# Optimization experiments

Hardware: AMD Instinct MI355X
Metric: run time of the kernel (lower is better)

The kernel has to match this reference:

```python
import jax, jax.numpy as jnp
import numpy as np

B, N = 4096, 64
EPS = 1e-6
LANE = np.array([13.55, 17.45, 21.12, 24.91], dtype=np.float32)


def _lin_params(key, out_f, in_f):
    k1, k2 = jax.random.split(key)
    bound = 1.0 / np.sqrt(in_f)
    W = jax.random.uniform(k1, (out_f, in_f), jnp.float32, -bound, bound)
    b = jax.random.uniform(k2, (out_f,), jnp.float32, -bound, bound)
    return W, b


def setup_inputs() -> dict:
    key = jax.random.key(0)
    ks = jax.random.split(key, 16)
    inp = {
        "ego_y": jax.random.uniform(ks[0], (B,), jnp.float32, 10.0, 28.0),
        "Pn": jax.random.normal(ks[1], (B, N, 2), jnp.float32),
        "Pego": jax.random.normal(ks[2], (B, 2), jnp.float32),
        "Vn": jax.random.normal(ks[3], (B, N, 2), jnp.float32),
        "Vego": jax.random.normal(ks[4], (B, 2), jnp.float32),
        "Cn": jax.random.normal(ks[5], (B, N, 2), jnp.float32),
    }
    inp["W_sel"], inp["b_sel"] = _lin_params(ks[6], 4, 4)
    inp["W_s0"], inp["b_s0"] = _lin_params(ks[7], 8, 4)      # aug_sin0
    inp["W_map"], inp["b_map"] = _lin_params(ks[8], 8, 48)   # Er map
    inp["W_efc"], inp["b_efc"] = _lin_params(ks[9], 2, 8)
    inp["W_s1"], inp["b_s1"] = _lin_params(ks[10], 17, 2)    # aug_sin1
    inp["W1"], inp["b1"] = _lin_params(ks[11], 256, 114)     # En_mlp
    inp["W2"], inp["b2"] = _lin_params(ks[12], 128, 256)
    inp["W3"], inp["b3"] = _lin_params(ks[13], 2, 128)
    inp["Ww"], inp["bw"] = _lin_params(ks[14], 1, 6)
    return inp


def _leaky(x):
    return jnp.where(x >= 0, x, 0.1 * x)


def _auge(data, W_sin, b_sin):
    # data: [..., d]; returns concat of 10 feature blocks along last axis
    sin = jnp.sin(data @ W_sin.T + b_sin) + EPS
    sqr = data ** 2 + EPS
    cub = data ** 3 + EPS
    exp = jnp.exp(data) + EPS
    inv = 1.0 / (data + EPS)
    return jnp.concatenate(
        [data, sin, sqr, cub, exp, inv, 1.0 / sin, 1.0 / sqr, 1.0 / cub, 1.0 / exp],
        axis=-1,
    )


def reference(ego_y, Pn, Pego, Vn, Vego, Cn,
              W_sel, b_sel, W_s0, b_s0, W_map, b_map, W_efc, b_efc,
              W_s1, b_s1, W1, b1, W2, b2, W3, b3, Ww, bw):
    lane = jnp.asarray(LANE)
    # ---- Er_net (batched over B) ----
    delta_y = lane[None, :] - ego_y[:, None]                      # [B,4]
    x = jax.nn.softmax(delta_y @ W_sel.T + b_sel, axis=-1) * delta_y
    x = _auge(x, W_s0, b_s0)                                      # [B,48]
    x = _leaky(x @ W_map.T + b_map)                               # [B,8]
    Er = x @ W_efc.T + b_efc                                      # [B,2]

    # ---- En_net (batched over B, vectorized over N neighbors) ----
    Pego_r = jnp.broadcast_to(Pego[:, None, :], (B, N, 2))
    Vego_r = jnp.broadcast_to(Vego[:, None, :], (B, N, 2))
    dP = Pn - Pego_r
    dV = Vn - Vego_r
    dP_aug = _auge(dP, W_s1, b_s1)                                # [B,N,50]
    dV_aug = _auge(dV, W_s1, b_s1)                                # [B,N,50]
    Ninfo = jnp.concatenate(
        [Pego_r, Pn, dP, dP_aug, Vego_r, Vn, dV, dV_aug, Cn], axis=-1
    )                                                             # [B,N,114]
    h = _leaky(Ninfo @ W1.T + b1)                                 # [B,N,256]
    h = _leaky(h @ W2.T + b2)                                     # [B,N,128]
    En = h @ W3.T + b3                                            # [B,N,2]
    logits = jnp.concatenate([En, Pn, dP], axis=-1) @ Ww.T + bw   # [B,N,1]
    weight = jax.nn.softmax(logits, axis=1)                       # softmax over neighbors
    En_out = jnp.sum(weight * En, axis=1)                         # [B,2]

    return jnp.concatenate([Er, En_out], axis=-1)                 # [B,4]
```

## Files before the change

kernel.cpp:

```cpp
#include <hip/hip_runtime.h>
#include <math.h>

#define EPS 1e-6f
#define NB 4096
#define NN 64

typedef __attribute__((ext_vector_type(8))) short short8_t;
typedef __attribute__((ext_vector_type(4))) short short4_t;
typedef __attribute__((ext_vector_type(4))) float f32x4;

__device__ __forceinline__ unsigned short f2bf(float x) {
  unsigned u = __float_as_uint(x);
  u = u + 0x7fffu + ((u >> 16) & 1u);
  return (unsigned short)(u >> 16);
}

__global__ __launch_bounds__(512)
void w_prep_kernel(const float* __restrict__ W1,
                   const float* __restrict__ W2,
                   short* __restrict__ W1F,
                   short* __restrict__ W2F) {
  __shared__ float S[32768];
  const int tid = threadIdx.x;
  if (blockIdx.x == 0) {
    for (int i = tid; i < 256 * 114; i += 512) S[i] = W1[i];
    __syncthreads();
    for (int u = tid; u < 4096; u += 512) {
      int l = u & 63, ks = (u >> 6) & 3, mt = u >> 8;
      int m = mt * 16 + (l & 15);
      int k0 = ks * 32 + (l >> 4) * 8;
      short8_t hi, lo;
#pragma unroll
      for (int j = 0; j < 8; j++) {
        int k = k0 + j;
        float x = (k < 114) ? S[m * 114 + k] : 0.0f;
        unsigned uu = __float_as_uint(x);
        hi[j] = (short)(unsigned short)(uu >> 16);
        lo[j] = (short)f2bf(x - __uint_as_float(uu & 0xFFFF0000u));
      }
      int base = ((mt * 4 + ks) * 64 + l) * 8;
      *(short8_t*)&W1F[base] = hi;
      *(short8_t*)&W1F[32768 + base] = lo;
    }
  } else {
    for (int i = tid; i < 128 * 256; i += 512) S[i] = W2[i];
    __syncthreads();
    for (int u = tid; u < 4096; u += 512) {
      int l = u & 63, ks = (u >> 6) & 7, mt = u >> 9;
      int m = mt * 16 + (l & 15);
      int k0 = ks * 32 + (l >> 4) * 8;
      short8_t hi, lo;
#pragma unroll
      for (int j = 0; j < 8; j++) {
        float x = S[m * 256 + k0 + j];
        unsigned uu = __float_as_uint(x);
        hi[j] = (short)(unsigned short)(uu >> 16);
        lo[j] = (short)f2bf(x - __uint_as_float(uu & 0xFFFF0000u));
      }
      int base = ((mt * 8 + ks) * 64 + l) * 8;
      *(short8_t*)&W2F[base] = hi;
      *(short8_t*)&W2F[32768 + base] = lo;
    }
  }
}

__global__ __launch_bounds__(512, 4)
void en_kernel(const float* __restrict__ Pn, const float* __restrict__ Pego,
               const float* __restrict__ Vn, const float* __restrict__ Vego,
               const float* __restrict__ Cn,
               const float* __restrict__ W_s1, const float* __restrict__ b_s1,
               const float* __restrict__ b1, const float* __restrict__ b2,
               const float* __restrict__ W3, const float* __restrict__ b3,
               const float* __restrict__ Ww, const float* __restrict__ bw,
               const float* __restrict__ ego_y,
               const float* __restrict__ W_sel, const float* __restrict__ b_sel,
               const float* __restrict__ W_s0, const float* __restrict__ b_s0,
               const float* __restrict__ W_map, const float* __restrict__ b_map,
               const float* __restrict__ W_efc, const float* __restrict__ b_efc,
               const short* __restrict__ W1F, const short* __restrict__ W2F,
               float* __restrict__ out) {
  __shared__ __align__(16) short uni[2][64 * 256];
  __shared__ float stash[4 * 64];
  __shared__ float w3s[256];
  __shared__ float en_part[4][64][2];

  const int b = blockIdx.x;
  const int tid = threadIdx.x;
  const int w = tid >> 6;
  const int l = tid & 63;
  const int lr = l & 15;
  const int lq = l >> 4;
  const int ntb = (w >> 2) * 2;

  if (tid < 256) w3s[tid] = W3[tid];

  {
    const int r = l;
    const int rsw = (r & 7) << 3;
    auto putg = [&](int g, const float* v) {
      short8_t hi, lo;
#pragma unroll
      for (int i = 0; i < 8; i++) {
        unsigned u = __float_as_uint(v[i]);
        hi[i] = (short)(unsigned short)(u >> 16);
        lo[i] = (short)f2bf(v[i] - __uint_as_float(u & 0xFFFF0000u));
      }
      int idx = r * 128 + ((g * 8) ^ rsw);
      *(short8_t*)&uni[0][idx] = hi;
      *(short8_t*)&uni[1][idx] = lo;
    };
    if (w == 6) {
      const float2 p2 = ((const float2*)Pn)[b * NN + r];
      float e0 = Pego[b * 2 + 0], e1 = Pego[b * 2 + 1];
      stash[0 * 64 + r] = p2.x; stash[1 * 64 + r] = p2.y;
      stash[2 * 64 + r] = p2.x - e0; stash[3 * 64 + r] = p2.y - e1;
      const float2 cn = ((const float2*)Cn)[b * NN + r];
      float g14[8] = {cn.x, cn.y, 0.f, 0.f, 0.f, 0.f, 0.f, 0.f};
      float g15[8] = {0.f, 0.f, 0.f, 0.f, 0.f, 0.f, 0.f, 0.f};
      putg(14, g14);
      putg(15, g15);
    } else if (w < 6) {
      const bool isV = (w >= 3);
      const int role = isV ? (w - 3) : w;
      const int gb = isV ? 7 : 0;
      const float2 p2 = ((const float2*)(isV ? Vn : Pn))[b * NN + r];
      const float* Eb = isV ? Vego : Pego;
      float e0 = Eb[b * 2 + 0], e1 = Eb[b * 2 + 1];
      float d0 = p2.x - e0, d1 = p2.y - e1;
      if (role == 0) {
        float a15 = fmaf(W_s1[30], d0, fmaf(W_s1[31], d1, b_s1[15]));
        float a16 = fmaf(W_s1[32], d0, fmaf(W_s1[33], d1, b_s1[16]));
        float s15 = sinf(a15) + EPS, s16 = sinf(a16) + EPS;
        float q0 = d0 * d0 + EPS, q1 = d1 * d1 + EPS;
        float c30 = (d0 * d0) * d0 + EPS, c31 = (d1 * d1) * d1 + EPS;
        float ex0 = expf(d0) + EPS, ex1 = expf(d1) + EPS;
        float g0[8] = {e0, e1, p2.x, p2.y, d0, d1, d0, d1};
        float g3[8] = {s16, q0, q1, c30, c31, ex0, ex1, 1.0f / (d0 + EPS)};
        float g6[8] = {1.0f / s15, 1.0f / s16, 1.0f / q0, 1.0f / q1,
                       1.0f / c30, 1.0f / c31, 1.0f / ex0, 1.0f / ex1};
        putg(gb + 0, g0);
        putg(gb + 3, g3);
        putg(gb + 6, g6);
      } else if (role == 1) {
        float s[8];
#pragma unroll
        for (int i = 0; i < 8; i++) {
          float a = fmaf(W_s1[2 * i], d0, fmaf(W_s1[2 * i + 1], d1, b_s1[i]));
          s[i] = sinf(a) + EPS;
        }
        float g1[8] = {s[0], s[1], s[2], s[3], s[4], s[5], s[6], s[7]};
        float g4[8] = {1.0f / (d1 + EPS), 1.0f / s[0], 1.0f / s[1], 1.0f / s[2],
                       1.0f / s[3], 1.0f / s[4], 1.0f / s[5], 1.0f / s[6]};
        putg(gb + 1, g1);
        putg(gb + 4, g4);
      } else {
        float s[9];
#pragma unroll
        for (int i = 0; i < 9; i++) {
          float a = fmaf(W_s1[2 * (7 + i)], d0,
                         fmaf(W_s1[2 * (7 + i) + 1], d1, b_s1[7 + i]));
          s[i] = sinf(a) + EPS;
        }
        float g2[8] = {s[1], s[2], s[3], s[4], s[5], s[6], s[7], s[8]};
        float g5[8] = {1.0f / s[0], 1.0f / s[1], 1.0f / s[2], 1.0f / s[3],
                       1.0f / s[4], 1.0f / s[5], 1.0f / s[6], 1.0f / s[7]};
        putg(gb + 2, g2);
        putg(gb + 5, g5);
      }
    } else if (l < 8) {
      const int sub = l;
      const float lane4[4] = {13.55f, 17.45f, 21.12f, 24.91f};
      float ego = ego_y[b];
      float dy[4];
#pragma unroll
      for (int j = 0; j < 4; j++) dy[j] = lane4[j] - ego;
      float t[4];
#pragma unroll
      for (int i = 0; i < 4; i++) {
        float a = b_sel[i];
#pragma unroll
        for (int j = 0; j < 4; j++) a = fmaf(W_sel[i * 4 + j], dy[j], a);
        t[i] = a;
      }
      float m = fmaxf(fmaxf(t[0], t[1]), fmaxf(t[2], t[3]));
      float e[4], s = 0.f;
#pragma unroll
      for (int i = 0; i < 4; i++) { e[i] = expf(t[i] - m); s += e[i]; }
      float x[4];
#pragma unroll
      for (int i = 0; i < 4; i++) x[i] = (e[i] / s) * dy[i];
      float f[48];
      float sn[8];
#pragma unroll
      for (int k = 0; k < 8; k++) {
        float a = b_s0[k];
#pragma unroll
        for (int j = 0; j < 4; j++) a = fmaf(W_s0[k * 4 + j], x[j], a);
        sn[k] = sinf(a) + EPS;
      }
#pragma unroll
      for (int i = 0; i < 4; i++) f[i] = x[i];
#pragma unroll
      for (int k = 0; k < 8; k++) f[4 + k] = sn[k];
#pragma unroll
      for (int i = 0; i < 4; i++) {
        float q = x[i] * x[i] + EPS;
        f[12 + i] = q; f[36 + i] = 1.0f / q;
      }
#pragma unroll
      for (int i = 0; i < 4; i++) {
        float c3 = (x[i] * x[i]) * x[i] + EPS;
        f[16 + i] = c3; f[40 + i] = 1.0f / c3;
      }
#pragma unroll
      for (int i = 0; i < 4; i++) {
        float ex = expf(x[i]) + EPS;
        f[20 + i] = ex; f[44 + i] = 1.0f / ex;
      }
#pragma unroll
      for (int i = 0; i < 4; i++) f[24 + i] = 1.0f / (x[i] + EPS);
#pragma unroll
      for (int k = 0; k < 8; k++) f[28 + k] = 1.0f / sn[k];
      float a = b_map[sub];
#pragma unroll
      for (int k = 0; k < 48; k++) a = fmaf(W_map[sub * 48 + k], f[k], a);
      float y = fmaxf(a, 0.1f * a);
      float t0 = W_efc[sub] * y;
      float t1 = W_efc[8 + sub] * y;
#pragma unroll
      for (int off = 4; off > 0; off >>= 1) {
        t0 += __shfl_xor(t0, off);
        t1 += __shfl_xor(t1, off);
      }
      if (sub == 0) {
        out[b * 4 + 0] = t0 + b_efc[0];
        out[b * 4 + 1] = t1 + b_efc[1];
      }
    }
  }
  __syncthreads();

  const short* w1b = W1F + (w & 3) * 4 * 4 * 512 + l * 8;
  f32x4 acc1[4][2];
#pragma unroll
  for (int m = 0; m < 4; m++)
#pragma unroll
    for (int n = 0; n < 2; n++) acc1[m][n] = (f32x4)0.0f;

#pragma unroll
  for (int ks = 0; ks < 4; ks++) {
    short8_t w1h[4], w1l[4];
#pragma unroll
    for (int m = 0; m < 4; m++) {
      w1h[m] = *(const short8_t*)&w1b[(m * 4 + ks) * 512];
      w1l[m] = *(const short8_t*)&w1b[32768 + (m * 4 + ks) * 512];
    }
    short8_t bh[2], bl[2];
#pragma unroll
    for (int n = 0; n < 2; n++) {
      int rr = (ntb + n) * 16 + lr;
      int idx = rr * 128 + ((ks * 32 + lq * 8) ^ ((rr & 7) << 3));
      bh[n] = *(const short8_t*)&uni[0][idx];
      bl[n] = *(const short8_t*)&uni[1][idx];
    }
    __builtin_amdgcn_s_setprio(1);
#pragma unroll
    for (int m = 0; m < 4; m++)
#pragma unroll
      for (int n = 0; n < 2; n++)
        acc1[m][n] = __builtin_amdgcn_mfma_f32_16x16x32_bf16(
            w1h[m], bh[n], acc1[m][n], 0, 0, 0);
#pragma unroll
    for (int m = 0; m < 4; m++)
#pragma unroll
      for (int n = 0; n < 2; n++)
        acc1[m][n] = __builtin_amdgcn_mfma_f32_16x16x32_bf16(
            w1h[m], bl[n], acc1[m][n], 0, 0, 0);
#pragma unroll
    for (int m = 0; m < 4; m++)
#pragma unroll
      for (int n = 0; n < 2; n++)
        acc1[m][n] = __builtin_amdgcn_mfma_f32_16x16x32_bf16(
            w1l[m], bh[n], acc1[m][n], 0, 0, 0);
    __builtin_amdgcn_s_setprio(0);
  }

  __syncthreads();

#pragma unroll
  for (int m = 0; m < 4; m++) {
    int o0 = ((w & 3) * 4 + m) * 16 + lq * 4;
    f32x4 bb = *(const f32x4*)&b1[o0];
#pragma unroll
    for (int n = 0; n < 2; n++) {
      int rr = (ntb + n) * 16 + lr;
      short4_t hq, lo4;
#pragma unroll
      for (int i = 0; i < 4; i++) {
        float v = acc1[m][n][i] + bb[i];
        v = fmaxf(v, 0.1f * v);
        unsigned u = __float_as_uint(v);
        hq[i] = (short)(unsigned short)(u >> 16);
        lo4[i] = (short)f2bf(v - __uint_as_float(u & 0xFFFF0000u));
      }
      int idx = rr * 256 + (o0 ^ ((rr & 7) << 3));
      *(short4_t*)&uni[0][idx] = hq;
      *(short4_t*)&uni[1][idx] = lo4;
    }
  }
  __syncthreads();

  const short* w2b = W2F + (w & 3) * 2 * 8 * 512 + l * 8;
  f32x4 acc2[2][2];
#pragma unroll
  for (int m = 0; m < 2; m++)
#pragma unroll
    for (int n = 0; n < 2; n++) acc2[m][n] = (f32x4)0.0f;

#pragma unroll
  for (int ks = 0; ks < 8; ks++) {
    short8_t w2h[2], w2l[2];
#pragma unroll
    for (int m = 0; m < 2; m++) {
      w2h[m] = *(const short8_t*)&w2b[(m * 8 + ks) * 512];
      w2l[m] = *(const short8_t*)&w2b[32768 + (m * 8 + ks) * 512];
    }
    short8_t bh[2], bl[2];
#pragma unroll
    for (int n = 0; n < 2; n++) {
      int rr = (ntb + n) * 16 + lr;
      int idx = rr * 256 + ((ks * 32 + lq * 8) ^ ((rr & 7) << 3));
      bh[n] = *(const short8_t*)&uni[0][idx];
      bl[n] = *(const short8_t*)&uni[1][idx];
    }
    __builtin_amdgcn_s_setprio(1);
#pragma unroll
    for (int m = 0; m < 2; m++)
#pragma unroll
      for (int n = 0; n < 2; n++)
        acc2[m][n] = __builtin_amdgcn_mfma_f32_16x16x32_bf16(
            w2h[m], bh[n], acc2[m][n], 0, 0, 0);
#pragma unroll
    for (int m = 0; m < 2; m++)
#pragma unroll
      for (int n = 0; n < 2; n++)
        acc2[m][n] = __builtin_amdgcn_mfma_f32_16x16x32_bf16(
            w2h[m], bl[n], acc2[m][n], 0, 0, 0);
#pragma unroll
    for (int m = 0; m < 2; m++)
#pragma unroll
      for (int n = 0; n < 2; n++)
        acc2[m][n] = __builtin_amdgcn_mfma_f32_16x16x32_bf16(
            w2l[m], bh[n], acc2[m][n], 0, 0, 0);
    __builtin_amdgcn_s_setprio(0);
  }

  {
    f32x4 w3v[2][2];
#pragma unroll
    for (int c = 0; c < 2; c++)
#pragma unroll
      for (int m = 0; m < 2; m++)
        w3v[c][m] = *(const f32x4*)
            &w3s[c * 128 + ((w & 3) * 2 + m) * 16 + lq * 4];

    float p00 = 0.f, p01 = 0.f, p10 = 0.f, p11 = 0.f;
#pragma unroll
    for (int m = 0; m < 2; m++) {
      int o0 = ((w & 3) * 2 + m) * 16 + lq * 4;
      f32x4 bb = *(const f32x4*)&b2[o0];
#pragma unroll
      for (int i = 0; i < 4; i++) {
        float u0 = acc2[m][0][i] + bb[i];
        u0 = fmaxf(u0, 0.1f * u0);
        float u1 = acc2[m][1][i] + bb[i];
        u1 = fmaxf(u1, 0.1f * u1);
        p00 = fmaf(u0, w3v[0][m][i], p00);
        p10 = fmaf(u0, w3v[1][m][i], p10);
        p01 = fmaf(u1, w3v[0][m][i], p01);
        p11 = fmaf(u1, w3v[1][m][i], p11);
      }
    }
#pragma unroll
    for (int off = 16; off < 64; off <<= 1) {
      p00 += __shfl_xor(p00, off);
      p01 += __shfl_xor(p01, off);
      p10 += __shfl_xor(p10, off);
      p11 += __shfl_xor(p11, off);
    }
    if (l < 16) {
      en_part[w & 3][ntb * 16 + l][0] = p00;
      en_part[w & 3][ntb * 16 + l][1] = p10;
      en_part[w & 3][(ntb + 1) * 16 + l][0] = p01;
      en_part[w & 3][(ntb + 1) * 16 + l][1] = p11;
    }
  }
  __syncthreads();

  if (tid < 64) {
    const int r = tid;
    float E0 = b3[0] + en_part[0][r][0] + en_part[1][r][0] +
               en_part[2][r][0] + en_part[3][r][0];
    float E1 = b3[1] + en_part[0][r][1] + en_part[1][r][1] +
               en_part[2][r][1] + en_part[3][r][1];
    float pn0 = stash[0 * 64 + r], pn1 = stash[1 * 64 + r];
    float dp0 = stash[2 * 64 + r], dp1 = stash[3 * 64 + r];
    float logit = bw[0];
    logit = fmaf(E0, Ww[0], logit);
    logit = fmaf(E1, Ww[1], logit);
    logit = fmaf(pn0, Ww[2], logit);
    logit = fmaf(pn1, Ww[3], logit);
    logit = fmaf(dp0, Ww[4], logit);
    logit = fmaf(dp1, Ww[5], logit);
    float m = logit;
#pragma unroll
    for (int off = 32; off > 0; off >>= 1) m = fmaxf(m, __shfl_xor(m, off));
    float e = expf(logit - m);
    float ssum = e;
#pragma unroll
    for (int off = 32; off > 0; off >>= 1) ssum += __shfl_xor(ssum, off);
    float wgt = e / ssum;
    float o0 = wgt * E0, o1 = wgt * E1;
#pragma unroll
    for (int off = 32; off > 0; off >>= 1) {
      o0 += __shfl_xor(o0, off);
      o1 += __shfl_xor(o1, off);
    }
    if (r == 0) {
      out[b * 4 + 2] = o0;
      out[b * 4 + 3] = o1;
    }
  }
}

extern "C" void kernel_launch(void* const* d_in, const int* in_sizes, int n_in,
                              void* d_out, int out_size, void* d_ws, size_t ws_size,
                              hipStream_t stream) {
  const float* ego_y = (const float*)d_in[0];
  const float* Pn    = (const float*)d_in[1];
  const float* Pego  = (const float*)d_in[2];
  const float* Vn    = (const float*)d_in[3];
  const float* Vego  = (const float*)d_in[4];
  const float* Cn    = (const float*)d_in[5];
  const float* W_sel = (const float*)d_in[6];
  const float* b_sel = (const float*)d_in[7];
  const float* W_s0  = (const float*)d_in[8];
  const float* b_s0  = (const float*)d_in[9];
  const float* W_map = (const float*)d_in[10];
  const float* b_map = (const float*)d_in[11];
  const float* W_efc = (const float*)d_in[12];
  const float* b_efc = (const float*)d_in[13];
  const float* W_s1  = (const float*)d_in[14];
  const float* b_s1  = (const float*)d_in[15];
  const float* W1    = (const float*)d_in[16];
  const float* b1    = (const float*)d_in[17];
  const float* W2    = (const float*)d_in[18];
  const float* b2    = (const float*)d_in[19];
  const float* W3    = (const float*)d_in[20];
  const float* b3    = (const float*)d_in[21];
  const float* Ww    = (const float*)d_in[22];
  const float* bw    = (const float*)d_in[23];
  float* out = (float*)d_out;

  short* W1F = (short*)d_ws;
  short* W2F = W1F + 65536;

  w_prep_kernel<<<2, 512, 0, stream>>>(W1, W2, W1F, W2F);
  en_kernel<<<NB, 512, 0, stream>>>(Pn, Pego, Vn, Vego, Cn, W_s1, b_s1,
                                    b1, b2, W3, b3, Ww, bw,
                                    ego_y, W_sel, b_sel, W_s0, b_s0,
                                    W_map, b_map, W_efc, b_efc,
                                    W1F, W2F, out);
}
```

Before: 218.0 us.

## Switch MLP GEMMs to 32x32x16 MFMA tiles and parallelize weight prep

Both hidden-layer GEMMs now use 32x32x16 bf16 MFMA instead of 16x16x32. Each wave handles a 32-row neighbor tile against 64 or 32 output features, and the weight fragment layout in the prep kernel is rebuilt to match. The prep kernel is split across 12 blocks instead of 2 so weight packing no longer serializes on two blocks. Biases b1/b2 are staged in shared memory, and the final reduction shrinks to one cross-half shuffle. The larger tiles cut LDS operand reads and MFMA instruction count, at the cost of larger accumulator register use.

Result: slower. 232.2 us (+6.5%).

```diff
diff --git a/kernel.cpp b/kernel.cpp
--- a/kernel.cpp
+++ b/kernel.cpp
@@ -8,6 +8,7 @@
 typedef __attribute__((ext_vector_type(8))) short short8_t;
 typedef __attribute__((ext_vector_type(4))) short short4_t;
 typedef __attribute__((ext_vector_type(4))) float f32x4;
+typedef __attribute__((ext_vector_type(16))) float f32x16;
 
 __device__ __forceinline__ unsigned short f2bf(float x) {
   unsigned u = __float_as_uint(x);
@@ -15,49 +16,53 @@
   return (unsigned short)(u >> 16);
 }
 
-__global__ __launch_bounds__(512)
+__global__ __launch_bounds__(256)
 void w_prep_kernel(const float* __restrict__ W1,
                    const float* __restrict__ W2,
                    short* __restrict__ W1F,
                    short* __restrict__ W2F) {
-  __shared__ float S[32768];
+  __shared__ float S[8192];
+  const int g = blockIdx.x;
   const int tid = threadIdx.x;
-  if (blockIdx.x == 0) {
-    for (int i = tid; i < 256 * 114; i += 512) S[i] = W1[i];
+  if (g < 8) {
+    for (int i = tid; i < 32 * 114; i += 256) S[i] = W1[g * 32 * 114 + i];
     __syncthreads();
-    for (int u = tid; u < 4096; u += 512) {
-      int l = u & 63, ks = (u >> 6) & 3, mt = u >> 8;
-      int m = mt * 16 + (l & 15);
-      int k0 = ks * 32 + (l >> 4) * 8;
+#pragma unroll
+    for (int it = 0; it < 2; it++) {
+      int u = tid + it * 256;
+      int l = u & 63, ks = u >> 6;
+      int lm = l & 31, k0 = ks * 16 + (l >> 5) * 8;
       short8_t hi, lo;
 #pragma unroll
       for (int j = 0; j < 8; j++) {
         int k = k0 + j;
-        float x = (k < 114) ? S[m * 114 + k] : 0.0f;
+        float x = (k < 114) ? S[lm * 114 + k] : 0.0f;
         unsigned uu = __float_as_uint(x);
         hi[j] = (short)(unsigned short)(uu >> 16);
         lo[j] = (short)f2bf(x - __uint_as_float(uu & 0xFFFF0000u));
       }
-      int base = ((mt * 4 + ks) * 64 + l) * 8;
+      int base = ((g * 8 + ks) * 64 + l) * 8;
       *(short8_t*)&W1F[base] = hi;
       *(short8_t*)&W1F[32768 + base] = lo;
     }
   } else {
-    for (int i = tid; i < 128 * 256; i += 512) S[i] = W2[i];
+    const int mt = g - 8;
+    for (int i = tid; i < 32 * 256; i += 256) S[i] = W2[mt * 32 * 256 + i];
     __syncthreads();
-    for (int u = tid; u < 4096; u += 512) {
-      int l = u & 63, ks = (u >> 6) & 7, mt = u >> 9;
-      int m = mt * 16 + (l & 15);
-      int k0 = ks * 32 + (l >> 4) * 8;
+#pragma unroll
+    for (int it = 0; it < 4; it++) {
+      int u = tid + it * 256;
+      int l = u & 63, ks = u >> 6;
+      int lm = l & 31, k0 = ks * 16 + (l >> 5) * 8;
       short8_t hi, lo;
 #pragma unroll
       for (int j = 0; j < 8; j++) {
-        float x = S[m * 256 + k0 + j];
+        float x = S[lm * 256 + k0 + j];
         unsigned uu = __float_as_uint(x);
         hi[j] = (short)(unsigned short)(uu >> 16);
         lo[j] = (short)f2bf(x - __uint_as_float(uu & 0xFFFF0000u));
       }
-      int base = ((mt * 8 + ks) * 64 + l) * 8;
+      int base = ((mt * 16 + ks) * 64 + l) * 8;
       *(short8_t*)&W2F[base] = hi;
       *(short8_t*)&W2F[32768 + base] = lo;
     }
@@ -82,17 +87,21 @@
   __shared__ __align__(16) short uni[2][64 * 256];
   __shared__ float stash[4 * 64];
   __shared__ float w3s[256];
+  __shared__ float b1s[256];
+  __shared__ float b2s[128];
   __shared__ float en_part[4][64][2];
 
   const int b = blockIdx.x;
   const int tid = threadIdx.x;
   const int w = tid >> 6;
   const int l = tid & 63;
-  const int lr = l & 15;
-  const int lq = l >> 4;
-  const int ntb = (w >> 2) * 2;
-
-  if (tid < 256) w3s[tid] = W3[tid];
+  const int lm = l & 31;
+  const int lh = l >> 5;
+  const int mg = w & 3;
+  const int nt = w >> 2;
+
+  if (tid < 256) { w3s[tid] = W3[tid]; b1s[tid] = b1[tid]; }
+  else if (tid < 384) b2s[tid - 256] = b2[tid - 256];
 
   {
     const int r = l;
@@ -240,159 +249,98 @@
   }
   __syncthreads();
 
-  const short* w1b = W1F + (w & 3) * 4 * 4 * 512 + l * 8;
-  f32x4 acc1[4][2];
-#pragma unroll
-  for (int m = 0; m < 4; m++)
-#pragma unroll
-    for (int n = 0; n < 2; n++) acc1[m][n] = (f32x4)0.0f;
-
-#pragma unroll
-  for (int ks = 0; ks < 4; ks++) {
-    short8_t w1h[4], w1l[4];
-#pragma unroll
-    for (int m = 0; m < 4; m++) {
-      w1h[m] = *(const short8_t*)&w1b[(m * 4 + ks) * 512];
-      w1l[m] = *(const short8_t*)&w1b[32768 + (m * 4 + ks) * 512];
-    }
-    short8_t bh[2], bl[2];
-#pragma unroll
-    for (int n = 0; n < 2; n++) {
-      int rr = (ntb + n) * 16 + lr;
-      int idx = rr * 128 + ((ks * 32 + lq * 8) ^ ((rr & 7) << 3));
-      bh[n] = *(const short8_t*)&uni[0][idx];
-      bl[n] = *(const short8_t*)&uni[1][idx];
-    }
+  const int rr = nt * 32 + lm;
+  const int rsw = (rr & 7) << 3;
+  f32x16 acc1[2];
+#pragma unroll
+  for (int m = 0; m < 2; m++) acc1[m] = (f32x16)0.0f;
+
+#pragma unroll
+  for (int ks = 0; ks < 8; ks++) {
+    short8_t w1h[2], w1l[2];
+#pragma unroll
+    for (int m = 0; m < 2; m++) {
+      int fo = (((mg * 2 + m) * 8 + ks) * 64 + l) * 8;
+      w1h[m] = *(const short8_t*)&W1F[fo];
+      w1l[m] = *(const short8_t*)&W1F[32768 + fo];
+    }
+    int idx = rr * 128 + ((ks * 16 + lh * 8) ^ rsw);
+    short8_t bh = *(const short8_t*)&uni[0][idx];
+    short8_t bl = *(const short8_t*)&uni[1][idx];
     __builtin_amdgcn_s_setprio(1);
 #pragma unroll
-    for (int m = 0; m < 4; m++)
-#pragma unroll
-      for (int n = 0; n < 2; n++)
-        acc1[m][n] = __builtin_amdgcn_mfma_f32_16x16x32_bf16(
-            w1h[m], bh[n], acc1[m][n], 0, 0, 0);
-#pragma unroll
-    for (int m = 0; m < 4; m++)
-#pragma unroll
-      for (int n = 0; n < 2; n++)
-        acc1[m][n] = __builtin_amdgcn_mfma_f32_16x16x32_bf16(
-            w1h[m], bl[n], acc1[m][n], 0, 0, 0);
-#pragma unroll
-    for (int m = 0; m < 4; m++)
-#pragma unroll
-      for (int n = 0; n < 2; n++)
-        acc1[m][n] = __builtin_amdgcn_mfma_f32_16x16x32_bf16(
-            w1l[m], bh[n], acc1[m][n], 0, 0, 0);
+    for (int m = 0; m < 2; m++)
+      acc1[m] = __builtin_amdgcn_mfma_f32_32x32x16_bf16(w1h[m], bh, acc1[m], 0, 0, 0);
+#pragma unroll
+    for (int m = 0; m < 2; m++)
+      acc1[m] = __builtin_amdgcn_mfma_f32_32x32x16_bf16(w1h[m], bl, acc1[m], 0, 0, 0);
+#pragma unroll
+    for (int m = 0; m < 2; m++)
+      acc1[m] = __builtin_amdgcn_mfma_f32_32x32x16_bf16(w1l[m], bh, acc1[m], 0, 0, 0);
     __builtin_amdgcn_s_setprio(0);
   }
 
   __syncthreads();
 
 #pragma unroll
-  for (int m = 0; m < 4; m++) {
-    int o0 = ((w & 3) * 4 + m) * 16 + lq * 4;
-    f32x4 bb = *(const f32x4*)&b1[o0];
-#pragma unroll
-    for (int n = 0; n < 2; n++) {
-      int rr = (ntb + n) * 16 + lr;
+  for (int m = 0; m < 2; m++) {
+#pragma unroll
+    for (int q = 0; q < 4; q++) {
+      int o0 = (mg * 2 + m) * 32 + q * 8 + lh * 4;
+      f32x4 bb = *(const f32x4*)&b1s[o0];
       short4_t hq, lo4;
 #pragma unroll
       for (int i = 0; i < 4; i++) {
-        float v = acc1[m][n][i] + bb[i];
+        float v = acc1[m][q * 4 + i] + bb[i];
         v = fmaxf(v, 0.1f * v);
         unsigned u = __float_as_uint(v);
         hq[i] = (short)(unsigned short)(u >> 16);
         lo4[i] = (short)f2bf(v - __uint_as_float(u & 0xFFFF0000u));
       }
-      int idx = rr * 256 + (o0 ^ ((rr & 7) << 3));
+      int idx = rr * 256 + (o0 ^ rsw);
       *(short4_t*)&uni[0][idx] = hq;
       *(short4_t*)&uni[1][idx] = lo4;
     }
   }
   __syncthreads();
 
-  const short* w2b = W2F + (w & 3) * 2 * 8 * 512 + l * 8;
-  f32x4 acc2[2][2];
-#pragma unroll
-  for (int m = 0; m < 2; m++)
-#pragma unroll
-    for (int n = 0; n < 2; n++) acc2[m][n] = (f32x4)0.0f;
-
-#pragma unroll
-  for (int ks = 0; ks < 8; ks++) {
-    short8_t w2h[2], w2l[2];
-#pragma unroll
-    for (int m = 0; m < 2; m++) {
-      w2h[m] = *(const short8_t*)&w2b[(m * 8 + ks) * 512];
-      w2l[m] = *(const short8_t*)&w2b[32768 + (m * 8 + ks) * 512];
-    }
-    short8_t bh[2], bl[2];
-#pragma unroll
-    for (int n = 0; n < 2; n++) {
-      int rr = (ntb + n) * 16 + lr;
-      int idx = rr * 256 + ((ks * 32 + lq * 8) ^ ((rr & 7) << 3));
-      bh[n] = *(const short8_t*)&uni[0][idx];
-      bl[n] = *(const short8_t*)&uni[1][idx];
-    }
+  f32x16 acc2 = (f32x16)0.0f;
+#pragma unroll
+  for (int ks = 0; ks < 16; ks++) {
+    int fo = ((mg * 16 + ks) * 64 + l) * 8;
+    short8_t w2h = *(const short8_t*)&W2F[fo];
+    short8_t w2l = *(const short8_t*)&W2F[32768 + fo];
+    int idx = rr * 256 + ((ks * 16 + lh * 8) ^ rsw);
+    short8_t bh = *(const short8_t*)&uni[0][idx];
+    short8_t bl = *(const short8_t*)&uni[1][idx];
     __builtin_amdgcn_s_setprio(1);
-#pragma unroll
-    for (int m = 0; m < 2; m++)
-#pragma unroll
-      for (int n = 0; n < 2; n++)
-        acc2[m][n] = __builtin_amdgcn_mfma_f32_16x16x32_bf16(
-            w2h[m], bh[n], acc2[m][n], 0, 0, 0);
-#pragma unroll
-    for (int m = 0; m < 2; m++)
-#pragma unroll
-      for (int n = 0; n < 2; n++)
-        acc2[m][n] = __builtin_amdgcn_mfma_f32_16x16x32_bf16(
-            w2h[m], bl[n], acc2[m][n], 0, 0, 0);
-#pragma unroll
-    for (int m = 0; m < 2; m++)
-#pragma unroll
-      for (int n = 0; n < 2; n++)
-        acc2[m][n] = __builtin_amdgcn_mfma_f32_16x16x32_bf16(
-            w2l[m], bh[n], acc2[m][n], 0, 0, 0);
+    acc2 = __builtin_amdgcn_mfma_f32_32x32x16_bf16(w2h, bh, acc2, 0, 0, 0);
+    acc2 = __builtin_amdgcn_mfma_f32_32x32x16_bf16(w2h, bl, acc2, 0, 0, 0);
+    acc2 = __builtin_amdgcn_mfma_f32_32x32x16_bf16(w2l, bh, acc2, 0, 0, 0);
     __builtin_amdgcn_s_setprio(0);
   }
 
   {
-    f32x4 w3v[2][2];
-#pragma unroll
-    for (int c = 0; c < 2; c++)
-#pragma unroll
-      for (int m = 0; m < 2; m++)
-        w3v[c][m] = *(const f32x4*)
-            &w3s[c * 128 + ((w & 3) * 2 + m) * 16 + lq * 4];
-
-    float p00 = 0.f, p01 = 0.f, p10 = 0.f, p11 = 0.f;
-#pragma unroll
-    for (int m = 0; m < 2; m++) {
-      int o0 = ((w & 3) * 2 + m) * 16 + lq * 4;
-      f32x4 bb = *(const f32x4*)&b2[o0];
-#pragma unroll
-      for (int i = 0; i < 4; i++) {
-        float u0 = acc2[m][0][i] + bb[i];
-        u0 = fmaxf(u0, 0.1f * u0);
-        float u1 = acc2[m][1][i] + bb[i];
-        u1 = fmaxf(u1, 0.1f * u1);
-        p00 = fmaf(u0, w3v[0][m][i], p00);
-        p10 = fmaf(u0, w3v[1][m][i], p10);
-        p01 = fmaf(u1, w3v[0][m][i], p01);
-        p11 = fmaf(u1, w3v[1][m][i], p11);
-      }
-    }
-#pragma unroll
-    for (int off = 16; off < 64; off <<= 1) {
-      p00 += __shfl_xor(p00, off);
-      p01 += __shfl_xor(p01, off);
-      p10 += __shfl_xor(p10, off);
-      p11 += __shfl_xor(p11, off);
-    }
-    if (l < 16) {
-      en_part[w & 3][ntb * 16 + l][0] = p00;
-      en_part[w & 3][ntb * 16 + l][1] = p10;
-      en_part[w & 3][(ntb + 1) * 16 + l][0] = p01;
-      en_part[w & 3][(ntb + 1) * 16 + l][1] = p11;
+    float p0 = 0.f, p1 = 0.f;
+#pragma unroll
+    for (int q = 0; q < 4; q++) {
+      int o0 = mg * 32 + q * 8 + lh * 4;
+      f32x4 bb = *(const f32x4*)&b2s[o0];
+      f32x4 w30 = *(const f32x4*)&w3s[o0];
+      f32x4 w31 = *(const f32x4*)&w3s[128 + o0];
+#pragma unroll
+      for (int i = 0; i < 4; i++) {
+        float u = acc2[q * 4 + i] + bb[i];
+        u = fmaxf(u, 0.1f * u);
+        p0 = fmaf(u, w30[i], p0);
+        p1 = fmaf(u, w31[i], p1);
+      }
+    }
+    p0 += __shfl_xor(p0, 32);
+    p1 += __shfl_xor(p1, 32);
+    if (lh == 0) {
+      en_part[mg][rr][0] = p0;
+      en_part[mg][rr][1] = p1;
     }
   }
   __syncthreads();
@@ -465,7 +413,7 @@
   short* W1F = (short*)d_ws;
   short* W2F = W1F + 65536;
 
-  w_prep_kernel<<<2, 512, 0, stream>>>(W1, W2, W1F, W2F);
+  w_prep_kernel<<<12, 256, 0, stream>>>(W1, W2, W1F, W2F);
   en_kernel<<<NB, 512, 0, stream>>>(Pn, Pego, Vn, Vego, Cn, W_s1, b_s1,
                                     b1, b2, W3, b3, Ww, bw,
                                     ego_y, W_sel, b_sel, W_s0, b_s0,
```

## Interleave hi/lo bf16 splits, use packed cvt, parallelize weight prep, stage biases in LDS

Applied to the files above, without the earlier changes.

Changes the hi/lo bf16 split to round-to-nearest via v_cvt_pk_bf16_f32 (hi now rounded, not truncated) and interleaves the hi and lo fragments in both the weight buffers and the LDS activation buffer. The weight-prep kernel moves from 2 large blocks to 128 single-wave blocks with no LDS staging. Biases b1/b2 are staged into LDS. This is meant to cut conversion instruction count, spread the prep kernel across more CUs, and improve locality of paired hi/lo loads, at the cost of a changed LDS stride pattern that could alter bank conflicts.

New measurement: 218.4 us. No clear change (+0.2%).

```diff
diff --git a/kernel.cpp b/kernel.cpp
--- a/kernel.cpp
+++ b/kernel.cpp
@@ -6,61 +6,63 @@
 #define NN 64
 
 typedef __attribute__((ext_vector_type(8))) short short8_t;
-typedef __attribute__((ext_vector_type(4))) short short4_t;
 typedef __attribute__((ext_vector_type(4))) float f32x4;
-
-__device__ __forceinline__ unsigned short f2bf(float x) {
-  unsigned u = __float_as_uint(x);
-  u = u + 0x7fffu + ((u >> 16) & 1u);
-  return (unsigned short)(u >> 16);
+typedef __attribute__((ext_vector_type(4))) unsigned u32x4;
+typedef __attribute__((ext_vector_type(2))) unsigned u32x2;
+
+__device__ __forceinline__ unsigned cvtpk(float a, float b) {
+  unsigned r;
+  asm("v_cvt_pk_bf16_f32 %0, %1, %2" : "=v"(r) : "v"(a), "v"(b));
+  return r;
 }
-
-__global__ __launch_bounds__(512)
+__device__ __forceinline__ unsigned split2(float a, float b, unsigned& lo) {
+  unsigned h = cvtpk(a, b);
+  float ra = __uint_as_float(h << 16);
+  float rb = __uint_as_float(h & 0xFFFF0000u);
+  lo = cvtpk(a - ra, b - rb);
+  return h;
+}
+
+__global__ __launch_bounds__(64)
 void w_prep_kernel(const float* __restrict__ W1,
                    const float* __restrict__ W2,
                    short* __restrict__ W1F,
                    short* __restrict__ W2F) {
-  __shared__ float S[32768];
-  const int tid = threadIdx.x;
-  if (blockIdx.x == 0) {
-    for (int i = tid; i < 256 * 114; i += 512) S[i] = W1[i];
-    __syncthreads();
-    for (int u = tid; u < 4096; u += 512) {
-      int l = u & 63, ks = (u >> 6) & 3, mt = u >> 8;
-      int m = mt * 16 + (l & 15);
-      int k0 = ks * 32 + (l >> 4) * 8;
-      short8_t hi, lo;
-#pragma unroll
-      for (int j = 0; j < 8; j++) {
-        int k = k0 + j;
-        float x = (k < 114) ? S[m * 114 + k] : 0.0f;
-        unsigned uu = __float_as_uint(x);
-        hi[j] = (short)(unsigned short)(uu >> 16);
-        lo[j] = (short)f2bf(x - __uint_as_float(uu & 0xFFFF0000u));
-      }
-      int base = ((mt * 4 + ks) * 64 + l) * 8;
-      *(short8_t*)&W1F[base] = hi;
-      *(short8_t*)&W1F[32768 + base] = lo;
-    }
+  const int g = blockIdx.x;
+  const int l = threadIdx.x;
+  float v[8];
+  if (g < 64) {
+    int mt = g >> 2, ks = g & 3;
+    int m = mt * 16 + (l & 15), k0 = ks * 32 + (l >> 4) * 8;
+#pragma unroll
+    for (int j = 0; j < 8; j++)
+      v[j] = (k0 + j < 114) ? W1[m * 114 + k0 + j] : 0.0f;
+    u32x4 hi, lo;
+#pragma unroll
+    for (int i = 0; i < 4; i++) {
+      unsigned lt;
+      hi[i] = split2(v[2 * i], v[2 * i + 1], lt);
+      lo[i] = lt;
+    }
+    int base = ((mt * 4 + ks) * 64 + l) * 16;
+    *(u32x4*)&W1F[base] = hi;
+    *(u32x4*)&W1F[base + 8] = lo;
   } else {
-    for (int i = tid; i < 128 * 256; i += 512) S[i] = W2[i];
-    __syncthreads();
-    for (int u = tid; u < 4096; u += 512) {
-      int l = u & 63, ks = (u >> 6) & 7, mt = u >> 9;
-      int m = mt * 16 + (l & 15);
-      int k0 = ks * 32 + (l >> 4) * 8;
-      short8_t hi, lo;
-#pragma unroll
-      for (int j = 0; j < 8; j++) {
-        float x = S[m * 256 + k0 + j];
-        unsigned uu = __float_as_uint(x);
-        hi[j] = (short)(unsigned short)(uu >> 16);
-        lo[j] = (short)f2bf(x - __uint_as_float(uu & 0xFFFF0000u));
-      }
-      int base = ((mt * 8 + ks) * 64 + l) * 8;
-      *(short8_t*)&W2F[base] = hi;
-      *(short8_t*)&W2F[32768 + base] = lo;
-    }
+    int t = g - 64;
+    int mt = t >> 3, ks = t & 7;
+    int m = mt * 16 + (l & 15), k0 = ks * 32 + (l >> 4) * 8;
+#pragma unroll
+    for (int j = 0; j < 8; j++) v[j] = W2[m * 256 + k0 + j];
+    u32x4 hi, lo;
+#pragma unroll
+    for (int i = 0; i < 4; i++) {
+      unsigned lt;
+      hi[i] = split2(v[2 * i], v[2 * i + 1], lt);
+      lo[i] = lt;
+    }
+    int base = ((mt * 8 + ks) * 64 + l) * 16;
+    *(u32x4*)&W2F[base] = hi;
+    *(u32x4*)&W2F[base + 8] = lo;
   }
 }
 
@@ -79,9 +81,11 @@
                const float* __restrict__ W_efc, const float* __restrict__ b_efc,
                const short* __restrict__ W1F, const short* __restrict__ W2F,
                float* __restrict__ out) {
-  __shared__ __align__(16) short uni[2][64 * 256];
+  __shared__ __align__(16) short uni[64 * 512];
   __shared__ float stash[4 * 64];
   __shared__ float w3s[256];
+  __shared__ float b1s[256];
+  __shared__ float b2s[128];
   __shared__ float en_part[4][64][2];
 
   const int b = blockIdx.x;
@@ -92,22 +96,23 @@
   const int lq = l >> 4;
   const int ntb = (w >> 2) * 2;
 
-  if (tid < 256) w3s[tid] = W3[tid];
+  if (tid < 256) { w3s[tid] = W3[tid]; b1s[tid] = b1[tid]; }
+  else if (tid < 384) b2s[tid - 256] = b2[tid - 256];
 
   {
     const int r = l;
     const int rsw = (r & 7) << 3;
     auto putg = [&](int g, const float* v) {
-      short8_t hi, lo;
-#pragma unroll
-      for (int i = 0; i < 8; i++) {
-        unsigned u = __float_as_uint(v[i]);
-        hi[i] = (short)(unsigned short)(u >> 16);
-        lo[i] = (short)f2bf(v[i] - __uint_as_float(u & 0xFFFF0000u));
-      }
-      int idx = r * 128 + ((g * 8) ^ rsw);
-      *(short8_t*)&uni[0][idx] = hi;
-      *(short8_t*)&uni[1][idx] = lo;
+      u32x4 hi, lo;
+#pragma unroll
+      for (int i = 0; i < 4; i++) {
+        unsigned lt;
+        hi[i] = split2(v[2 * i], v[2 * i + 1], lt);
+        lo[i] = lt;
+      }
+      int idx = r * 256 + ((g * 8) ^ rsw);
+      *(u32x4*)&uni[idx] = hi;
+      *(u32x4*)&uni[idx + 128] = lo;
     };
     if (w == 6) {
       const float2 p2 = ((const float2*)Pn)[b * NN + r];
@@ -240,7 +245,7 @@
   }
   __syncthreads();
 
-  const short* w1b = W1F + (w & 3) * 4 * 4 * 512 + l * 8;
+  const short* w1b = W1F + l * 16;
   f32x4 acc1[4][2];
 #pragma unroll
   for (int m = 0; m < 4; m++)
@@ -252,16 +257,17 @@
     short8_t w1h[4], w1l[4];
 #pragma unroll
     for (int m = 0; m < 4; m++) {
-      w1h[m] = *(const short8_t*)&w1b[(m * 4 + ks) * 512];
-      w1l[m] = *(const short8_t*)&w1b[32768 + (m * 4 + ks) * 512];
+      int fo = (((w & 3) * 4 + m) * 4 + ks) * 1024;
+      w1h[m] = *(const short8_t*)&w1b[fo];
+      w1l[m] = *(const short8_t*)&w1b[fo + 8];
     }
     short8_t bh[2], bl[2];
 #pragma unroll
     for (int n = 0; n < 2; n++) {
       int rr = (ntb + n) * 16 + lr;
-      int idx = rr * 128 + ((ks * 32 + lq * 8) ^ ((rr & 7) << 3));
-      bh[n] = *(const short8_t*)&uni[0][idx];
-      bl[n] = *(const short8_t*)&uni[1][idx];
+      int idx = rr * 256 + ((ks * 32 + lq * 8) ^ ((rr & 7) << 3));
+      bh[n] = *(const short8_t*)&uni[idx];
+      bl[n] = *(const short8_t*)&uni[idx + 128];
     }
     __builtin_amdgcn_s_setprio(1);
 #pragma unroll
@@ -290,27 +296,28 @@
 #pragma unroll
   for (int m = 0; m < 4; m++) {
     int o0 = ((w & 3) * 4 + m) * 16 + lq * 4;
-    f32x4 bb = *(const f32x4*)&b1[o0];
+    f32x4 bb = *(const f32x4*)&b1s[o0];
 #pragma unroll
     for (int n = 0; n < 2; n++) {
       int rr = (ntb + n) * 16 + lr;
-      short4_t hq, lo4;
-#pragma unroll
-      for (int i = 0; i < 4; i++) {
-        float v = acc1[m][n][i] + bb[i];
-        v = fmaxf(v, 0.1f * v);
-        unsigned u = __float_as_uint(v);
-        hq[i] = (short)(unsigned short)(u >> 16);
-        lo4[i] = (short)f2bf(v - __uint_as_float(u & 0xFFFF0000u));
-      }
-      int idx = rr * 256 + (o0 ^ ((rr & 7) << 3));
-      *(short4_t*)&uni[0][idx] = hq;
-      *(short4_t*)&uni[1][idx] = lo4;
+      float v0 = fmaxf(acc1[m][n][0] + bb[0], 0.1f * (acc1[m][n][0] + bb[0]));
+      float v1 = fmaxf(acc1[m][n][1] + bb[1], 0.1f * (acc1[m][n][1] + bb[1]));
+      float v2 = fmaxf(acc1[m][n][2] + bb[2], 0.1f * (acc1[m][n][2] + bb[2]));
+      float v3 = fmaxf(acc1[m][n][3] + bb[3], 0.1f * (acc1[m][n][3] + bb[3]));
+      u32x2 hi, lo;
+      unsigned l0, l1;
+      hi[0] = split2(v0, v1, l0);
+      hi[1] = split2(v2, v3, l1);
+      lo[0] = l0;
+      lo[1] = l1;
+      int idx = rr * 512 + (o0 ^ ((rr & 7) << 3));
+      *(u32x2*)&uni[idx] = hi;
+      *(u32x2*)&uni[idx + 256] = lo;
     }
   }
   __syncthreads();
 
-  const short* w2b = W2F + (w & 3) * 2 * 8 * 512 + l * 8;
+  const short* w2b = W2F + l * 16;
   f32x4 acc2[2][2];
 #pragma unroll
   for (int m = 0; m < 2; m++)
@@ -322,16 +329,17 @@
     short8_t w2h[2], w2l[2];
 #pragma unroll
     for (int m = 0; m < 2; m++) {
-      w2h[m] = *(const short8_t*)&w2b[(m * 8 + ks) * 512];
-      w2l[m] = *(const short8_t*)&w2b[32768 + (m * 8 + ks) * 512];
+      int fo = (((w & 3) * 2 + m) * 8 + ks) * 1024;
+      w2h[m] = *(const short8_t*)&w2b[fo];
+      w2l[m] = *(const short8_t*)&w2b[fo + 8];
     }
     short8_t bh[2], bl[2];
 #pragma unroll
     for (int n = 0; n < 2; n++) {
       int rr = (ntb + n) * 16 + lr;
-      int idx = rr * 256 + ((ks * 32 + lq * 8) ^ ((rr & 7) << 3));
-      bh[n] = *(const short8_t*)&uni[0][idx];
-      bl[n] = *(const short8_t*)&uni[1][idx];
+      int idx = rr * 512 + ((ks * 32 + lq * 8) ^ ((rr & 7) << 3));
+      bh[n] = *(const short8_t*)&uni[idx];
+      bl[n] = *(const short8_t*)&uni[idx + 256];
     }
     __builtin_amdgcn_s_setprio(1);
 #pragma unroll
@@ -368,7 +376,7 @@
 #pragma unroll
     for (int m = 0; m < 2; m++) {
       int o0 = ((w & 3) * 2 + m) * 16 + lq * 4;
-      f32x4 bb = *(const f32x4*)&b2[o0];
+      f32x4 bb = *(const f32x4*)&b2s[o0];
 #pragma unroll
       for (int i = 0; i < 4; i++) {
         float u0 = acc2[m][0][i] + bb[i];
@@ -465,7 +473,7 @@
   short* W1F = (short*)d_ws;
   short* W2F = W1F + 65536;
 
-  w_prep_kernel<<<2, 512, 0, stream>>>(W1, W2, W1F, W2F);
+  w_prep_kernel<<<128, 64, 0, stream>>>(W1, W2, W1F, W2F);
   en_kernel<<<NB, 512, 0, stream>>>(Pn, Pego, Vn, Vego, Cn, W_s1, b_s1,
                                     b1, b2, W3, b3, Ww, bw,
                                     ego_y, W_sel, b_sel, W_s0, b_s0,
```
